# Kernel tuning notes

Measured on AMD Instinct MI355X. Metric: run time of the kernel, lower is better.

## Reference

```python
import jax, jax.numpy as jnp
import numpy as np

B, N, DIM = 4, 2048, 1024
HEAD = 16
INTER = 1024
HD = INTER // HEAD  # 64
SCALE = INTER ** (-0.5)


def setup_inputs() -> dict:
    key = jax.random.key(0)
    k1, k2, k3 = jax.random.split(key, 3)
    features = jax.random.normal(k1, (B, N, DIM), dtype=jnp.float32)
    W_qkv = jax.random.normal(k2, (DIM, 3 * INTER), dtype=jnp.float32) * (DIM ** -0.5)
    W_out = jax.random.normal(k3, (INTER, DIM), dtype=jnp.float32) * (INTER ** -0.5)
    return {"features": features, "W_qkv": W_qkv, "W_out": W_out}


def reference(features, W_qkv, W_out):
    # fc_qkv: [b, n, 3*inter], chunk into q, k, v
    qkv = jnp.einsum('bnd,de->bne', features, W_qkv)
    q, k, v = jnp.split(qkv, 3, axis=-1)
    # b n (h d) -> b n h d
    q = q.reshape(B, N, HEAD, HD)
    k = k.reshape(B, N, HEAD, HD)
    v = v.reshape(B, N, HEAD, HD)
    # scores: b h i j  (scale = inter_dim ** -0.5, as in source)
    alpha = jnp.einsum('bihd,bjhd->bhij', q, k) * SCALE
    att = jax.nn.softmax(alpha, axis=-1)
    out = jnp.einsum('bhij,bjhd->bihd', att, v)
    out = out.reshape(B, N, INTER)
    # fc_out (dropout_ratio=0.0 -> identity)
    return jnp.einsum('bni,id->bnd', out, W_out)
```

## Files before the change

kernel.cpp:

```cpp
#include <hip/hip_runtime.h>
#include <stdint.h>

#define BB 4
#define SEQ 2048
#define DMODEL 1024
#define NHEAD 16
#define HDIM 64
#define INTER 1024
#define QSCALE 0.045084220027780106f

#if __has_builtin(__builtin_amdgcn_exp2f)
#define EXP2F(x) __builtin_amdgcn_exp2f(x)
#else
#define EXP2F(x) exp2f(x)
#endif

typedef unsigned short u16;
typedef __attribute__((ext_vector_type(4))) unsigned short u16x4;
typedef __attribute__((ext_vector_type(4))) short s16x4;
typedef __attribute__((ext_vector_type(8))) short s16x8;
typedef __attribute__((ext_vector_type(4))) float f32x4;
typedef __attribute__((ext_vector_type(16))) float f32x16;
typedef __attribute__((ext_vector_type(4))) unsigned int u32x4;

__device__ __forceinline__ u16 f2bf(float f) {
  unsigned int u = __float_as_uint(f);
  u += 0x7FFFu + ((u >> 16) & 1u);
  return (u16)(u >> 16);
}

#if __has_builtin(__builtin_amdgcn_cvt_pk_bf16_f32)
typedef __attribute__((ext_vector_type(2))) __bf16 bf16x2_t;
__device__ __forceinline__ unsigned int pk2bf(float a, float b) {
  bf16x2_t r = __builtin_amdgcn_cvt_pk_bf16_f32(a, b);
  return *reinterpret_cast<unsigned int*>(&r);
}
#else
__device__ __forceinline__ unsigned int pk2bf(float a, float b) {
  return (unsigned int)f2bf(a) | ((unsigned int)f2bf(b) << 16);
}
#endif

__device__ __forceinline__ void async16(const u16* g, u16* l) {
  __builtin_amdgcn_global_load_lds((__attribute__((address_space(1))) void*)(void*)(g),
                                   (__attribute__((address_space(3))) void*)(l),
                                   16, 0, 0);
}

__device__ __forceinline__ void make_pb(const unsigned int* cc, int half,
                                        s16x8& pb0, s16x8& pb1) {
#if __has_builtin(__builtin_amdgcn_permlane32_swap)
  (void)half;
  auto r02 = __builtin_amdgcn_permlane32_swap(cc[0], cc[2], false, false);
  auto r13 = __builtin_amdgcn_permlane32_swap(cc[1], cc[3], false, false);
  auto r46 = __builtin_amdgcn_permlane32_swap(cc[4], cc[6], false, false);
  auto r57 = __builtin_amdgcn_permlane32_swap(cc[5], cc[7], false, false);
  u32x4 w0 = {(unsigned)r02[0], (unsigned)r13[0], (unsigned)r02[1], (unsigned)r13[1]};
  u32x4 w1 = {(unsigned)r46[0], (unsigned)r57[0], (unsigned)r46[1], (unsigned)r57[1]};
#else
  unsigned x0 = __shfl_xor((int)cc[0], 32, 64), x1 = __shfl_xor((int)cc[1], 32, 64);
  unsigned x2 = __shfl_xor((int)cc[2], 32, 64), x3 = __shfl_xor((int)cc[3], 32, 64);
  unsigned x4 = __shfl_xor((int)cc[4], 32, 64), x5 = __shfl_xor((int)cc[5], 32, 64);
  unsigned x6 = __shfl_xor((int)cc[6], 32, 64), x7 = __shfl_xor((int)cc[7], 32, 64);
  u32x4 w0 = {half ? x2 : cc[0], half ? x3 : cc[1],
              half ? cc[2] : x0, half ? cc[3] : x1};
  u32x4 w1 = {half ? x6 : cc[4], half ? x7 : cc[5],
              half ? cc[6] : x4, half ? cc[7] : x5};
#endif
  pb0 = *reinterpret_cast<s16x8*>(&w0);
  pb1 = *reinterpret_cast<s16x8*>(&w1);
}

__global__ __launch_bounds__(256) void prep(
    const float* __restrict__ f, const float* __restrict__ wqkv,
    const float* __restrict__ wout, u16* __restrict__ Xb,
    u16* __restrict__ WqkvT, u16* __restrict__ WoutT) {
  __shared__ float tile[32][33];
  const int bid = blockIdx.x, tid = threadIdx.x;
  if (bid < 8192) {
    int i = (bid * 256 + tid) * 4;
    f32x4 v = *reinterpret_cast<const f32x4*>(f + i);
    uint2 o;
    o.x = pk2bf(v[0], v[1]);
    o.y = pk2bf(v[2], v[3]);
    *reinterpret_cast<uint2*>(Xb + i) = o;
  } else {
    const float* src; u16* dst; int rows, cols, bx, by;
    if (bid < 8192 + 3072) {
      int t = bid - 8192;
      src = wqkv; dst = WqkvT; rows = DMODEL; cols = 3 * INTER;
      bx = t % 96; by = t / 96;
    } else {
      int t = bid - 11264;
      src = wout; dst = WoutT; rows = INTER; cols = DMODEL;
      bx = t & 31; by = t >> 5;
    }
    int c0 = bx * 32, r0 = by * 32, tx = tid & 31, ty = tid >> 5;
    #pragma unroll
    for (int i = ty; i < 32; i += 8) tile[i][tx] = src[(size_t)(r0 + i) * cols + c0 + tx];
    __syncthreads();
    #pragma unroll
    for (int i = ty; i < 32; i += 8)
      dst[(size_t)(c0 + i) * rows + r0 + tx] = f2bf(tile[tx][i]);
  }
}

template <int MODE>
__global__ __launch_bounds__(256, 2) void gemm_bt(
    const u16* __restrict__ A, const u16* __restrict__ BT,
    float* __restrict__ Cf, u16* __restrict__ Qb, u16* __restrict__ Kp,
    u16* __restrict__ Vp, int K, int ldc) {
  __shared__ u16 As[128 * 32];
  __shared__ u16 Bs[128 * 32];
  const int tid = threadIdx.x;
  const int wave = tid >> 6, lane = tid & 63;
  const int row0 = blockIdx.y * 128, col0 = blockIdx.x * 128;
  const int wr = (wave >> 1) * 64, wc = (wave & 1) * 64;
  const int r = lane & 15, q8 = (lane >> 4) * 8;

  f32x4 acc[4][4] = {};

  const int sRow = lane >> 2, sK = (lane & 3) * 8;
  const u16* Ag0 = A + (size_t)(row0 + wave * 32 + sRow) * K + sK;
  const u16* Ag1 = Ag0 + (size_t)16 * K;
  const u16* Bg0 = BT + (size_t)(col0 + wave * 32 + sRow) * K + sK;
  const u16* Bg1 = Bg0 + (size_t)16 * K;
  u16* Al0 = &As[wave * 1024];
  u16* Al1 = Al0 + 512;
  u16* Bl0 = &Bs[wave * 1024];
  u16* Bl1 = Bl0 + 512;

  for (int k0 = 0; k0 < K; k0 += 32) {
    async16(Ag0 + k0, Al0);
    async16(Ag1 + k0, Al1);
    async16(Bg0 + k0, Bl0);
    async16(Bg1 + k0, Bl1);
    __syncthreads();
    s16x8 af[4], bf[4];
    #pragma unroll
    for (int t = 0; t < 4; t++) {
      af[t] = *reinterpret_cast<const s16x8*>(&As[(wr + t * 16 + r) * 32 + q8]);
      bf[t] = *reinterpret_cast<const s16x8*>(&Bs[(wc + t * 16 + r) * 32 + q8]);
    }
    #pragma unroll
    for (int i = 0; i < 4; i++)
      #pragma unroll
      for (int j = 0; j < 4; j++)
        acc[i][j] = __builtin_amdgcn_mfma_f32_16x16x32_bf16(af[i], bf[j], acc[i][j], 0, 0, 0);
    __syncthreads();
  }

  const int quad = lane >> 4;
  #pragma unroll
  for (int i = 0; i < 4; i++) {
    const int n = row0 + wr + i * 16 + quad * 4;
    const int b = n >> 11, nn = n & (SEQ - 1);
    #pragma unroll
    for (int j = 0; j < 4; j++) {
      const int gc = col0 + wc + j * 16 + r;
      if (MODE == 1) {
        #pragma unroll
        for (int reg = 0; reg < 4; reg++)
          Cf[(size_t)(n + reg) * ldc + gc] = acc[i][j][reg];
      } else if (gc < INTER) {
        size_t base = (size_t)n * INTER + gc;
        #pragma unroll
        for (int reg = 0; reg < 4; reg++)
          Qb[base + (size_t)reg * INTER] = f2bf(acc[i][j][reg] * QSCALE);
      } else if (gc < 2 * INTER) {
        int dim = gc - INTER, h = dim >> 6, d = dim & 63;
        int bh = b * NHEAD + h;
        size_t base = (((size_t)(bh * 64 + (nn >> 5)) * 4 + (d >> 4)) * 64 +
                       ((((d >> 3) & 1) << 5) | (nn & 31))) * 8 + (d & 7);
        #pragma unroll
        for (int reg = 0; reg < 4; reg++)
          Kp[base + reg * 8] = f2bf(acc[i][j][reg]);
      } else {
        int dim = gc - 2 * INTER, h = dim >> 6, d = dim & 63;
        int bh = b * NHEAD + h;
        size_t base = ((((size_t)(bh * 64 + (nn >> 5)) * 2 + ((nn >> 4) & 1)) * 2 +
                        (d >> 5)) * 64 +
                       ((((nn >> 3) & 1) << 5) | (d & 31))) * 8 + (nn & 7);
        uint2 pk;
        pk.x = pk2bf(acc[i][j][0], acc[i][j][1]);
        pk.y = pk2bf(acc[i][j][2], acc[i][j][3]);
        *reinterpret_cast<uint2*>(Vp + base) = pk;
      }
    }
  }
}

#define PSTEP(JCUR, SCUR, SNXT, KNXT, KPF)                                        \
  {                                                                               \
    s16x8 vf[4];                                                                  \
    _Pragma("unroll")                                                             \
    for (int c = 0; c < 4; c++)                                                   \
      vf[c] = *reinterpret_cast<const s16x8*>(vpb + (JCUR) * 2048 + c * 512);     \
    const int jpf = ((JCUR) + 2) & 63;                                            \
    _Pragma("unroll")                                                             \
    for (int c = 0; c < 4; c++)                                                   \
      KPF[c] = *reinterpret_cast<const s16x8*>(kpb + jpf * 2048 + c * 512);       \
    SNXT = (f32x16){};                                                            \
    __builtin_amdgcn_s_setprio(1);                                                \
    _Pragma("unroll")                                                             \
    for (int c = 0; c < 4; c++)                                                   \
      SNXT = __builtin_amdgcn_mfma_f32_32x32x16_bf16(KNXT[c], qf[c], SNXT, 0, 0, 0); \
    __builtin_amdgcn_s_setprio(0);                                                \
    unsigned int cc[8];                                                           \
    _Pragma("unroll")                                                             \
    for (int q = 0; q < 4; q++) {                                                 \
      float p0 = EXP2F(SCUR[q * 4 + 0]), p1 = EXP2F(SCUR[q * 4 + 1]);             \
      float p2 = EXP2F(SCUR[q * 4 + 2]), p3 = EXP2F(SCUR[q * 4 + 3]);             \
      ls += (p0 + p1) + (p2 + p3);                                                \
      cc[q * 2 + 0] = pk2bf(p0, p1);                                              \
      cc[q * 2 + 1] = pk2bf(p2, p3);                                              \
    }                                                                             \
    s16x8 pb0, pb1;                                                               \
    make_pb(cc, half, pb0, pb1);                                                  \
    __builtin_amdgcn_s_setprio(1);                                                \
    ot0 = __builtin_amdgcn_mfma_f32_32x32x16_bf16(vf[0], pb0, ot0, 0, 0, 0);      \
    ot1 = __builtin_amdgcn_mfma_f32_32x32x16_bf16(vf[1], pb0, ot1, 0, 0, 0);      \
    ot0 = __builtin_amdgcn_mfma_f32_32x32x16_bf16(vf[2], pb1, ot0, 0, 0, 0);      \
    ot1 = __builtin_amdgcn_mfma_f32_32x32x16_bf16(vf[3], pb1, ot1, 0, 0, 0);      \
    __builtin_amdgcn_s_setprio(0);                                                \
  }

__global__ __launch_bounds__(64, 3) void attn_kernel(
    const u16* __restrict__ Qb, const u16* __restrict__ Kp,
    const u16* __restrict__ Vp, u16* __restrict__ AO) {
  const int lane = threadIdx.x;
  const int l31 = lane & 31, half = lane >> 5;
  const int bh = blockIdx.x, b = bh >> 4, h = bh & 15;
  const int i0 = blockIdx.y * 32;

  const u16* qbase = Qb + (size_t)(b * SEQ + i0 + l31) * INTER + h * HDIM + half * 8;
  s16x8 qf[4];
  #pragma unroll
  for (int c = 0; c < 4; c++) qf[c] = *reinterpret_cast<const s16x8*>(qbase + c * 16);

  const u16* kpb = Kp + (size_t)bh * (64 * 4 * 512) + lane * 8;
  const u16* vpb = Vp + (size_t)bh * (64 * 4 * 512) + lane * 8;

  f32x16 ot0 = {}, ot1 = {};
  float ls = 0.f;

  s16x8 kX[4], kY[4];
  #pragma unroll
  for (int c = 0; c < 4; c++)
    kX[c] = *reinterpret_cast<const s16x8*>(kpb + 0 * 2048 + c * 512);
  f32x16 stA = {}, stB;
  #pragma unroll
  for (int c = 0; c < 4; c++)
    stA = __builtin_amdgcn_mfma_f32_32x32x16_bf16(kX[c], qf[c], stA, 0, 0, 0);
  #pragma unroll
  for (int c = 0; c < 4; c++)
    kY[c] = *reinterpret_cast<const s16x8*>(kpb + 1 * 2048 + c * 512);

  for (int jb = 0; jb < 64; jb += 2) {
    PSTEP(jb,     stA, stB, kY, kX)
    PSTEP(jb + 1, stB, stA, kX, kY)
  }

  ls += __shfl_xor(ls, 32, 64);
  float rinv = 1.0f / ls;

  u16* orow = AO + (size_t)(b * SEQ + i0 + l31) * INTER + h * HDIM;
  #pragma unroll
  for (int dt = 0; dt < 2; dt++) {
    const f32x16& o = dt ? ot1 : ot0;
    #pragma unroll
    for (int q = 0; q < 4; q++) {
      uint2 pk;
      pk.x = pk2bf(o[q * 4 + 0] * rinv, o[q * 4 + 1] * rinv);
      pk.y = pk2bf(o[q * 4 + 2] * rinv, o[q * 4 + 3] * rinv);
      *reinterpret_cast<uint2*>(orow + dt * 32 + q * 8 + half * 4) = pk;
    }
  }
}

extern "C" void kernel_launch(void* const* d_in, const int* in_sizes, int n_in,
                              void* d_out, int out_size, void* d_ws, size_t ws_size,
                              hipStream_t stream) {
  const float* features = (const float*)d_in[0];
  const float* W_qkv    = (const float*)d_in[1];
  const float* W_out    = (const float*)d_in[2];
  float* out = (float*)d_out;
  char* w = (char*)d_ws;
  u16* Xb    = (u16*)(w);
  u16* WqkvT = (u16*)(w + 16777216);
  u16* WoutT = (u16*)(w + 23068672);
  u16* Qb    = (u16*)(w + 25165824);
  u16* Kp    = (u16*)(w + 41943040);
  u16* Vp    = (u16*)(w + 58720256);
  u16* AO    = (u16*)(w + 75497472);

  prep<<<dim3(12288), dim3(256), 0, stream>>>(features, W_qkv, W_out, Xb, WqkvT, WoutT);
  gemm_bt<0><<<dim3(24, 64), dim3(256), 0, stream>>>(Xb, WqkvT, nullptr, Qb, Kp, Vp,
                                                     DMODEL, 0);
  attn_kernel<<<dim3(64, 64), dim3(64), 0, stream>>>(Qb, Kp, Vp, AO);
  gemm_bt<1><<<dim3(8, 64), dim3(256), 0, stream>>>(AO, WoutT, out, nullptr, nullptr,
                                                    nullptr, INTER, DMODEL);
}
```

Baseline: 275.0 us.

## Double-buffer LDS tiles in GEMM to overlap async loads with MFMA

The GEMM main loop now uses two LDS buffers for the A and B tiles. The next K-slice is issued with async global-to-LDS copies while MFMAs run on the current buffer, so each iteration needs one barrier instead of two. The aim is to hide global memory latency behind compute. LDS use doubles to 32 KB per block, which could reduce occupancy, and correctness depends on async16 completing before each barrier.

New measurement: 274.7 us. About the same (-0.1%).

```diff
diff --git a/kernel.cpp b/kernel.cpp
--- a/kernel.cpp
+++ b/kernel.cpp
@@ -105,13 +105,28 @@
   }
 }
 
+#define GCOMP(ABUF, BBUF)                                                         \
+  {                                                                               \
+    s16x8 af[4], bf[4];                                                           \
+    _Pragma("unroll")                                                             \
+    for (int t = 0; t < 4; t++) {                                                 \
+      af[t] = *reinterpret_cast<const s16x8*>(&ABUF[(wr + t * 16 + r) * 32 + q8]); \
+      bf[t] = *reinterpret_cast<const s16x8*>(&BBUF[(wc + t * 16 + r) * 32 + q8]); \
+    }                                                                             \
+    _Pragma("unroll")                                                             \
+    for (int i = 0; i < 4; i++)                                                   \
+      _Pragma("unroll")                                                           \
+      for (int j = 0; j < 4; j++)                                                 \
+        acc[i][j] = __builtin_amdgcn_mfma_f32_16x16x32_bf16(af[i], bf[j], acc[i][j], 0, 0, 0); \
+  }
+
 template <int MODE>
 __global__ __launch_bounds__(256, 2) void gemm_bt(
     const u16* __restrict__ A, const u16* __restrict__ BT,
     float* __restrict__ Cf, u16* __restrict__ Qb, u16* __restrict__ Kp,
     u16* __restrict__ Vp, int K, int ldc) {
-  __shared__ u16 As[128 * 32];
-  __shared__ u16 Bs[128 * 32];
+  __shared__ u16 As[2][128 * 32];
+  __shared__ u16 Bs[2][128 * 32];
   const int tid = threadIdx.x;
   const int wave = tid >> 6, lane = tid & 63;
   const int row0 = blockIdx.y * 128, col0 = blockIdx.x * 128;
@@ -125,28 +140,33 @@
   const u16* Ag1 = Ag0 + (size_t)16 * K;
   const u16* Bg0 = BT + (size_t)(col0 + wave * 32 + sRow) * K + sK;
   const u16* Bg1 = Bg0 + (size_t)16 * K;
-  u16* Al0 = &As[wave * 1024];
-  u16* Al1 = Al0 + 512;
-  u16* Bl0 = &Bs[wave * 1024];
-  u16* Bl1 = Bl0 + 512;
-
-  for (int k0 = 0; k0 < K; k0 += 32) {
-    async16(Ag0 + k0, Al0);
-    async16(Ag1 + k0, Al1);
-    async16(Bg0 + k0, Bl0);
-    async16(Bg1 + k0, Bl1);
+  u16* Al0a = &As[0][wave * 1024]; u16* Al1a = Al0a + 512;
+  u16* Bl0a = &Bs[0][wave * 1024]; u16* Bl1a = Bl0a + 512;
+  u16* Al0b = &As[1][wave * 1024]; u16* Al1b = Al0b + 512;
+  u16* Bl0b = &Bs[1][wave * 1024]; u16* Bl1b = Bl0b + 512;
+
+  async16(Ag0, Al0a);
+  async16(Ag1, Al1a);
+  async16(Bg0, Bl0a);
+  async16(Bg1, Bl1a);
+  __syncthreads();
+
+  for (int k0 = 0; k0 < K; k0 += 64) {
+    if (k0 + 32 < K) {
+      async16(Ag0 + k0 + 32, Al0b);
+      async16(Ag1 + k0 + 32, Al1b);
+      async16(Bg0 + k0 + 32, Bl0b);
+      async16(Bg1 + k0 + 32, Bl1b);
+    }
+    GCOMP(As[0], Bs[0])
     __syncthreads();
-    s16x8 af[4], bf[4];
-    #pragma unroll
-    for (int t = 0; t < 4; t++) {
-      af[t] = *reinterpret_cast<const s16x8*>(&As[(wr + t * 16 + r) * 32 + q8]);
-      bf[t] = *reinterpret_cast<const s16x8*>(&Bs[(wc + t * 16 + r) * 32 + q8]);
-    }
-    #pragma unroll
-    for (int i = 0; i < 4; i++)
-      #pragma unroll
-      for (int j = 0; j < 4; j++)
-        acc[i][j] = __builtin_amdgcn_mfma_f32_16x16x32_bf16(af[i], bf[j], acc[i][j], 0, 0, 0);
+    if (k0 + 64 < K) {
+      async16(Ag0 + k0 + 64, Al0a);
+      async16(Ag1 + k0 + 64, Al1a);
+      async16(Bg0 + k0 + 64, Bl0a);
+      async16(Bg1 + k0 + 64, Bl1a);
+    }
+    GCOMP(As[1], Bs[1])
     __syncthreads();
   }
 
```
